# Optimization experiments

Measured on AMD Instinct MI355X. Metric: run time of the kernel, lower is better.

Reference implementation:

```python
import jax, jax.numpy as jnp
import numpy as np

B, H, N, M = 8192, 512, 1024, 128
EPS_COS = 1e-8   # torch cosine_similarity default eps
EPS_NORM = 1e-16 # normalization eps in forward


def _linear_params(key, fan_in, fan_out):
    # torch nn.Linear default init: U(-1/sqrt(fan_in), 1/sqrt(fan_in))
    lim = 1.0 / np.sqrt(fan_in)
    kw, kb = jax.random.split(key)
    W = jax.random.uniform(kw, (fan_out, fan_in), minval=-lim, maxval=lim, dtype=jnp.float32)
    b = jax.random.uniform(kb, (fan_out,), minval=-lim, maxval=lim, dtype=jnp.float32)
    return W, b


def setup_inputs() -> dict:
    key = jax.random.key(0)
    ks = jax.random.split(key, 8)
    Wk, bk = _linear_params(ks[0], H, M)
    Wb, bb = _linear_params(ks[1], H, 1)
    Wg, bg = _linear_params(ks[2], H, 1)
    Ws, bs = _linear_params(ks[3], H, N)
    Wgam, bgam = _linear_params(ks[4], H, 1)
    x = jax.random.normal(ks[5], (B, H), dtype=jnp.float32)
    # previous_state is an attention-weight vector over memory rows (sums to 1)
    previous_state = jax.nn.softmax(jax.random.normal(ks[6], (B, N), dtype=jnp.float32), axis=-1)
    memory = jax.random.normal(ks[7], (N, M), dtype=jnp.float32)
    return dict(x=x, previous_state=previous_state, memory=memory,
                Wk=Wk, bk=bk, Wb=Wb, bb=bb, Wg=Wg, bg=bg,
                Ws=Ws, bs=bs, Wgam=Wgam, bgam=bgam)


def _circular_convolution(w, s):
    # Full circular convolution over the memory axis:
    #   out[b, i] = sum_j w[b, j] * s[b, (i - j) mod N]
    # Implemented via FFT to avoid materializing a [B, N, N] shift matrix.
    out = jnp.fft.irfft(jnp.fft.rfft(w, axis=-1) * jnp.fft.rfft(s, axis=-1),
                        n=w.shape[-1], axis=-1)
    # conv of nonnegative weights is nonnegative; clamp tiny FFT round-off
    # negatives so the fractional power below stays well defined.
    return jnp.maximum(out, 0.0)


def reference(x, previous_state, memory, Wk, bk, Wb, bb, Wg, bg, Ws, bs, Wgam, bgam):
    k = x @ Wk.T + bk                                   # [B, M]
    beta = jax.nn.softplus(x @ Wb.T + bb)               # [B, 1]
    g = jax.nn.sigmoid(x @ Wg.T + bg)                   # [B, 1]
    s = jax.nn.softmax(x @ Ws.T + bs, axis=-1)          # [B, N]
    gamma = 1.0 + jax.nn.softplus(x @ Wgam.T + bgam)    # [B, 1]

    # cosine similarity between each key and each memory row -> [B, N]
    k_n = k / jnp.maximum(jnp.linalg.norm(k, axis=-1, keepdims=True), EPS_COS)
    m_n = memory / jnp.maximum(jnp.linalg.norm(memory, axis=-1, keepdims=True), EPS_COS)
    cos = k_n @ m_n.T                                   # [B, N]

    w_c = jax.nn.softmax(beta * cos, axis=1)            # content addressing
    w_g = g * w_c + (1.0 - g) * previous_state          # interpolation gate
    w_t = _circular_convolution(w_g, s)                 # location shift
    w = w_t ** gamma                                    # sharpening
    w = w / (jnp.sum(w, axis=1, keepdims=True) + EPS_NORM)

    read = w @ memory                                   # [B, M]
    return read, w
```

## Files before the change

kernel.cpp:

```cpp
#include <hip/hip_runtime.h>
#include <hip/hip_bf16.h>

typedef __attribute__((ext_vector_type(8))) short short8;
typedef __attribute__((ext_vector_type(4))) short short4v;
typedef __attribute__((ext_vector_type(4))) float f32x4;

#define B_ROWS 8192
#define HDIM 512
#define NDIM 1024
#define MDIM 128

__device__ __forceinline__ float softplusf(float z) {
  return fmaxf(z, 0.f) + log1pf(__expf(-fabsf(z)));
}
__device__ __forceinline__ unsigned short f2bfu(float f) {
  __hip_bfloat16 h = __float2bfloat16(f);
  return *reinterpret_cast<unsigned short*>(&h);
}
__device__ __forceinline__ short8 pack8(float4 a, float4 b) {
  short8 r;
  r[0] = (short)f2bfu(a.x); r[1] = (short)f2bfu(a.y);
  r[2] = (short)f2bfu(a.z); r[3] = (short)f2bfu(a.w);
  r[4] = (short)f2bfu(b.x); r[5] = (short)f2bfu(b.y);
  r[6] = (short)f2bfu(b.z); r[7] = (short)f2bfu(b.w);
  return r;
}
__device__ __forceinline__ int pad(int i) { return i + (i >> 4); }

__global__ __launch_bounds__(256) void prep_all(
    const float* __restrict__ x, const float* __restrict__ Ws,
    const float* __restrict__ Wk, const float* __restrict__ mem,
    const float* __restrict__ Wb, const float* __restrict__ bb,
    const float* __restrict__ Wg, const float* __restrict__ bg,
    const float* __restrict__ Wgam, const float* __restrict__ bgam,
    short* __restrict__ xb, short* __restrict__ wsb, short* __restrict__ wkb,
    short* __restrict__ mn_bf, short* __restrict__ memT_bf,
    float* __restrict__ bgg)
{
  const int blk = blockIdx.x, t = threadIdx.x;
  if (blk < 512) {
    __shared__ float sredp[4];
    const int half = t >> 7, tl = t & 127;
    const int n = blk * 2 + half;
    const int wid = t >> 6;
    const float v = mem[n * MDIM + tl];
    float ss = v * v;
#pragma unroll
    for (int o = 32; o; o >>= 1) ss += __shfl_xor(ss, o);
    if ((t & 63) == 0) sredp[wid] = ss;
    __syncthreads();
    const float inv = 1.f / fmaxf(sqrtf(sredp[half * 2] + sredp[half * 2 + 1]), 1e-8f);
    mn_bf[n * MDIM + tl] = (short)f2bfu(v * inv);
    memT_bf[(size_t)tl * NDIM + n] = (short)f2bfu(v);
  } else if (blk < 2560) {
    const int wid = t >> 6, lane = t & 63;
    const int b = (blk - 512) * 4 + wid;
    const size_t xo = (size_t)b * HDIM + lane * 8;
    const float4 x0 = *(const float4*)(x + xo);
    const float4 x1 = *(const float4*)(x + xo + 4);
    const float4 b0 = *(const float4*)(Wb + lane * 8);
    const float4 b1 = *(const float4*)(Wb + lane * 8 + 4);
    const float4 g0 = *(const float4*)(Wg + lane * 8);
    const float4 g1 = *(const float4*)(Wg + lane * 8 + 4);
    const float4 m0 = *(const float4*)(Wgam + lane * 8);
    const float4 m1 = *(const float4*)(Wgam + lane * 8 + 4);
    float zb = x0.x*b0.x + x0.y*b0.y + x0.z*b0.z + x0.w*b0.w
             + x1.x*b1.x + x1.y*b1.y + x1.z*b1.z + x1.w*b1.w;
    float zg = x0.x*g0.x + x0.y*g0.y + x0.z*g0.z + x0.w*g0.w
             + x1.x*g1.x + x1.y*g1.y + x1.z*g1.z + x1.w*g1.w;
    float zm = x0.x*m0.x + x0.y*m0.y + x0.z*m0.z + x0.w*m0.w
             + x1.x*m1.x + x1.y*m1.y + x1.z*m1.z + x1.w*m1.w;
#pragma unroll
    for (int o = 32; o; o >>= 1) {
      zb += __shfl_xor(zb, o); zg += __shfl_xor(zg, o); zm += __shfl_xor(zm, o);
    }
    if (lane == 0) {
      zb += bb[0]; zg += bg[0]; zm += bgam[0];
      bgg[b * 4 + 0] = softplusf(zb);
      bgg[b * 4 + 1] = 1.f / (1.f + __expf(-zg));
      bgg[b * 4 + 2] = 1.f + softplusf(zm);
    }
  } else {
    const int NX = B_ROWS * HDIM / 4;
    const int NS = NDIM * HDIM / 4;
    const int NK = MDIM * HDIM / 4;
    const int stride = 1024 * 256;
    for (int i = (blk - 2560) * 256 + t; i < NX + NS + NK; i += stride) {
      const float* src; short* dst; int j = i;
      if (j < NX) { src = x; dst = xb; }
      else if (j < NX + NS) { j -= NX; src = Ws; dst = wsb; }
      else { j -= NX + NS; src = Wk; dst = wkb; }
      const float4 v = ((const float4*)src)[j];
      short4v o;
      o[0] = (short)f2bfu(v.x); o[1] = (short)f2bfu(v.y);
      o[2] = (short)f2bfu(v.z); o[3] = (short)f2bfu(v.w);
      ((short4v*)dst)[j] = o;
    }
  }
}

__global__ __launch_bounds__(256) void kgemm_norm(
    const short* __restrict__ xb, const short* __restrict__ wkb,
    const float* __restrict__ bk, short* __restrict__ khat)
{
  __shared__ __align__(16) short sA[32][40];
  __shared__ __align__(16) short sW[128][40];
  __shared__ float snorm[4][32];
  __shared__ float sinv[32];

  const int tid = threadIdx.x, lane = tid & 63, wid = tid >> 6;
  const int bm = blockIdx.x;
  const int fr = lane & 15, kg = (lane >> 4) << 3;

  f32x4 acc[2][2] = {};

  for (int k0 = 0; k0 < HDIM; k0 += 32) {
    if (k0) __syncthreads();
    if (tid < 128) {
      const int row = tid >> 2, c0 = (tid & 3) * 8;
      *(short8*)(&sA[row][c0]) =
          *(const short8*)(xb + (size_t)(bm * 32 + row) * HDIM + k0 + c0);
    }
#pragma unroll
    for (int u = tid; u < 512; u += 256) {
      const int row = u >> 2, c0 = (u & 3) * 8;
      *(short8*)(&sW[row][c0]) =
          *(const short8*)(wkb + (size_t)row * HDIM + k0 + c0);
    }
    __syncthreads();

    short8 af[2], bf[2];
#pragma unroll
    for (int i = 0; i < 2; i++) af[i] = *(const short8*)(&sA[i * 16 + fr][kg]);
#pragma unroll
    for (int n = 0; n < 2; n++) bf[n] = *(const short8*)(&sW[wid * 32 + n * 16 + fr][kg]);
#pragma unroll
    for (int i = 0; i < 2; i++)
#pragma unroll
      for (int n = 0; n < 2; n++)
        acc[i][n] = __builtin_amdgcn_mfma_f32_16x16x32_bf16(af[i], bf[n], acc[i][n], 0, 0, 0);
  }

  const int rbase = (lane >> 4) << 2;
  float z[2][2][4];
#pragma unroll
  for (int i = 0; i < 2; i++)
#pragma unroll
    for (int n = 0; n < 2; n++) {
      const float bv = bk[wid * 32 + n * 16 + fr];
#pragma unroll
      for (int r = 0; r < 4; r++) z[i][n][r] = acc[i][n][r] + bv;
    }
#pragma unroll
  for (int i = 0; i < 2; i++)
#pragma unroll
    for (int r = 0; r < 4; r++) {
      float sq = z[i][0][r] * z[i][0][r] + z[i][1][r] * z[i][1][r];
      sq += __shfl_xor(sq, 1); sq += __shfl_xor(sq, 2);
      sq += __shfl_xor(sq, 4); sq += __shfl_xor(sq, 8);
      if (fr == 0) snorm[wid][i * 16 + rbase + r] = sq;
    }
  __syncthreads();
  if (tid < 32) {
    const float nn = snorm[0][tid] + snorm[1][tid] + snorm[2][tid] + snorm[3][tid];
    sinv[tid] = 1.f / fmaxf(sqrtf(nn), 1e-8f);
  }
  __syncthreads();
#pragma unroll
  for (int i = 0; i < 2; i++)
#pragma unroll
    for (int n = 0; n < 2; n++)
#pragma unroll
      for (int r = 0; r < 4; r++) {
        const int grl = i * 16 + rbase + r;
        khat[(size_t)(bm * 32 + grl) * MDIM + wid * 32 + n * 16 + fr] =
            (short)f2bfu(z[i][n][r] * sinv[grl]);
      }
}

template<bool AF32, bool WF32>
__global__ __launch_bounds__(256) void gemm_bt(
    const void* __restrict__ Av, const void* __restrict__ Wv,
    const float* __restrict__ bias, float* __restrict__ C,
    int ncols, int K)
{
  __shared__ __align__(16) short sA[64][40];
  __shared__ __align__(16) short sW[64][40];

  const int tid = threadIdx.x;
  const int bm = blockIdx.y, bn = blockIdx.x;
  const int lrow = tid >> 2;
  const int lcol = (tid & 3) << 3;
  const int wid = tid >> 6, lane = tid & 63;
  const int wr = wid >> 1, wc = wid & 1;
  const int fr = lane & 15, kg = (lane >> 4) << 3;

  f32x4 acc[2][2] = {};

  const size_t arow = (size_t)(bm * 64 + lrow) * K + lcol;
  const size_t wrow = (size_t)(bn * 64 + lrow) * K + lcol;

  for (int k0 = 0; k0 < K; k0 += 32) {
    if constexpr (AF32) {
      const float* A = (const float*)Av;
      const float4 a0 = *(const float4*)(A + arow + k0);
      const float4 a1 = *(const float4*)(A + arow + k0 + 4);
      *(short8*)(&sA[lrow][lcol]) = pack8(a0, a1);
    } else {
      const short* A = (const short*)Av;
      *(short8*)(&sA[lrow][lcol]) = *(const short8*)(A + arow + k0);
    }
    if constexpr (WF32) {
      const float* W = (const float*)Wv;
      const float4 w0 = *(const float4*)(W + wrow + k0);
      const float4 w1 = *(const float4*)(W + wrow + k0 + 4);
      *(short8*)(&sW[lrow][lcol]) = pack8(w0, w1);
    } else {
      const short* W = (const short*)Wv;
      *(short8*)(&sW[lrow][lcol]) = *(const short8*)(W + wrow + k0);
    }
    __syncthreads();

    short8 af[2], bf[2];
#pragma unroll
    for (int i = 0; i < 2; i++) af[i] = *(const short8*)(&sA[wr * 32 + i * 16 + fr][kg]);
#pragma unroll
    for (int n = 0; n < 2; n++) bf[n] = *(const short8*)(&sW[wc * 32 + n * 16 + fr][kg]);

#pragma unroll
    for (int i = 0; i < 2; i++)
#pragma unroll
      for (int n = 0; n < 2; n++)
        acc[i][n] = __builtin_amdgcn_mfma_f32_16x16x32_bf16(af[i], bf[n], acc[i][n], 0, 0, 0);
    __syncthreads();
  }

#pragma unroll
  for (int i = 0; i < 2; i++)
#pragma unroll
    for (int n = 0; n < 2; n++) {
      const int gr = bm * 64 + wr * 32 + i * 16 + ((lane >> 4) << 2);
      const int gc = bn * 64 + wc * 32 + n * 16 + fr;
      const float bv = bias ? bias[gc] : 0.f;
#pragma unroll
      for (int r = 0; r < 4; r++)
        C[(size_t)(gr + r) * ncols + gc] = acc[i][n][r] + bv;
    }
}

template<bool AF32, bool WF32>
__global__ __launch_bounds__(256) void kgemm128(
    const void* __restrict__ Av, const void* __restrict__ Wv,
    const float* __restrict__ bias, float* __restrict__ C,
    int ncols, int K)
{
  __shared__ __align__(16) short sA[128 * 32];
  __shared__ __align__(16) short sB[128 * 32];

  const int tid = threadIdx.x, lane = tid & 63, wid = tid >> 6;
  const int bm = blockIdx.y, bn = blockIdx.x;
  const int wr = wid >> 1, wc = wid & 1;
  const int fr = lane & 15, kg = (lane >> 4) << 3;

  f32x4 acc[4][4] = {};

  for (int k0 = 0; k0 < K; k0 += 32) {
    if (k0) __syncthreads();

    if constexpr (AF32) {
      const float* A = (const float*)Av;
      const int row = tid >> 1, c0 = (tid & 1) * 16;
      const float* src = A + (size_t)(bm * 128 + row) * K + k0 + c0;
      const float4 v0 = *(const float4*)src;
      const float4 v1 = *(const float4*)(src + 4);
      const float4 v2 = *(const float4*)(src + 8);
      const float4 v3 = *(const float4*)(src + 12);
      short* d = &sA[row * 32 + c0];
      *(short8*)d = pack8(v0, v1);
      *(short8*)(d + 8) = pack8(v2, v3);
    } else {
      const short* A = (const short*)Av;
#pragma unroll
      for (int j = 0; j < 2; j++) {
        const int c = tid + j * 256;
        const short* g = A + (size_t)(bm * 128 + (c >> 2)) * K + k0 + (c & 3) * 8;
        short* l = &sA[(j * 256 + wid * 64) * 8];
        __builtin_amdgcn_global_load_lds(
            (const __attribute__((address_space(1))) void*)g,
            (__attribute__((address_space(3))) void*)l, 16, 0, 0);
      }
    }

    if constexpr (WF32) {
      const float* W = (const float*)Wv;
      const int row = tid >> 1, c0 = (tid & 1) * 16;
      const float* src = W + (size_t)(bn * 128 + row) * K + k0 + c0;
      const float4 v0 = *(const float4*)src;
      const float4 v1 = *(const float4*)(src + 4);
      const float4 v2 = *(const float4*)(src + 8);
      const float4 v3 = *(const float4*)(src + 12);
      short* d = &sB[row * 32 + c0];
      *(short8*)d = pack8(v0, v1);
      *(short8*)(d + 8) = pack8(v2, v3);
    } else {
      const short* W = (const short*)Wv;
#pragma unroll
      for (int j = 0; j < 2; j++) {
        const int c = tid + j * 256;
        const short* g = W + (size_t)(bn * 128 + (c >> 2)) * K + k0 + (c & 3) * 8;
        short* l = &sB[(j * 256 + wid * 64) * 8];
        __builtin_amdgcn_global_load_lds(
            (const __attribute__((address_space(1))) void*)g,
            (__attribute__((address_space(3))) void*)l, 16, 0, 0);
      }
    }
    __syncthreads();

    short8 af[4], bf[4];
#pragma unroll
    for (int m = 0; m < 4; m++)
      af[m] = *(const short8*)(&sA[(wr * 64 + m * 16 + fr) * 32 + kg]);
#pragma unroll
    for (int n = 0; n < 4; n++)
      bf[n] = *(const short8*)(&sB[(wc * 64 + n * 16 + fr) * 32 + kg]);

#pragma unroll
    for (int m = 0; m < 4; m++)
#pragma unroll
      for (int n = 0; n < 4; n++)
        acc[m][n] = __builtin_amdgcn_mfma_f32_16x16x32_bf16(af[m], bf[n], acc[m][n], 0, 0, 0);
  }

#pragma unroll
  for (int m = 0; m < 4; m++)
#pragma unroll
    for (int n = 0; n < 4; n++) {
      const int gr = bm * 128 + wr * 64 + m * 16 + ((lane >> 4) << 2);
      const int gc = bn * 128 + wc * 64 + n * 16 + fr;
      const float bv = bias ? bias[gc] : 0.f;
#pragma unroll
      for (int r = 0; r < 4; r++)
        C[(size_t)(gr + r) * ncols + gc] = acc[m][n][r] + bv;
    }
}

#define ANG0 (-0.0061359231515425650f)

template<int ST>
__device__ __forceinline__ void fft_mid(const float* __restrict__ sr,
                                        const float* __restrict__ si,
                                        float* __restrict__ dr,
                                        float* __restrict__ di, int tid,
                                        int j0, int j1, int j2, int j3)
{
  const int ls = 2 * ST, s = 1 << ls;
  const int p = tid >> ls, q = tid & (s - 1), tb = tid & ~(s - 1);
  const float a0r = sr[j0], a0i = si[j0], a1r = sr[j1], a1i = si[j1];
  const float a2r = sr[j2], a2i = si[j2], a3r = sr[j3], a3i = si[j3];
  const float b0r = a0r + a2r, b0i = a0i + a2i, b1r = a1r + a3r, b1i = a1i + a3i;
  const float b2r = a0r - a2r, b2i = a0i - a2i, b3r = a1r - a3r, b3i = a1i - a3i;
  const float A0r = b0r + b1r, A0i = b0i + b1i;
  const float A1r = b2r + b3i, A1i = b2i - b3r;
  const float A2r = b0r - b1r, A2i = b0i - b1i;
  const float A3r = b2r - b3i, A3i = b2i + b3r;
  const int o = q + 4 * s * p;
  dr[pad(o)] = A0r; di[pad(o)] = A0i;
  if constexpr (ST < 4) {
    float s1, c1; __sincosf(ANG0 * (float)tb, &s1, &c1);
    const float c2 = c1 * c1 - s1 * s1, s2 = 2.f * s1 * c1;
    const float c3 = c1 * c2 - s1 * s2, s3 = s1 * c2 + c1 * s2;
    dr[pad(o + s)]     = A1r * c1 - A1i * s1; di[pad(o + s)]     = A1r * s1 + A1i * c1;
    dr[pad(o + 2 * s)] = A2r * c2 - A2i * s2; di[pad(o + 2 * s)] = A2r * s2 + A2i * c2;
    dr[pad(o + 3 * s)] = A3r * c3 - A3i * s3; di[pad(o + 3 * s)] = A3r * s3 + A3i * c3;
  } else {
    dr[pad(o + s)]     = A1r; di[pad(o + s)]     = A1i;
    dr[pad(o + 2 * s)] = A2r; di[pad(o + 2 * s)] = A2i;
    dr[pad(o + 3 * s)] = A3r; di[pad(o + 3 * s)] = A3i;
  }
  __syncthreads();
}

template<int J>
__device__ __forceinline__ void fft512_mid(const float* __restrict__ sr,
                                           const float* __restrict__ si,
                                           float* __restrict__ dr,
                                           float* __restrict__ di, int tid)
{
  if (tid < 128) {
    constexpr int s  = (J == 1) ? 2 : (J == 2) ? 8 : 32;
    constexpr int ns = (J == 1) ? 256 : (J == 2) ? 64 : 16;
    constexpr int ls = (J == 1) ? 1 : (J == 2) ? 3 : 5;
    const int p = tid >> ls, q = tid & (s - 1);
    const float a0r = sr[pad(tid)],       a0i = si[pad(tid)];
    const float a1r = sr[pad(tid + 128)], a1i = si[pad(tid + 128)];
    const float a2r = sr[pad(tid + 256)], a2i = si[pad(tid + 256)];
    const float a3r = sr[pad(tid + 384)], a3i = si[pad(tid + 384)];
    const float b0r = a0r + a2r, b0i = a0i + a2i, b1r = a1r + a3r, b1i = a1i + a3i;
    const float b2r = a0r - a2r, b2i = a0i - a2i, b3r = a1r - a3r, b3i = a1i - a3i;
    const float A0r = b0r + b1r, A0i = b0i + b1i;
    const float A1r = b2r + b3i, A1i = b2i - b3r;
    const float A2r = b0r - b1r, A2i = b0i - b1i;
    const float A3r = b2r - b3i, A3i = b2i + b3r;
    float s1, c1; __sincosf((-6.283185307179586f / (float)ns) * (float)p, &s1, &c1);
    const float c2 = c1 * c1 - s1 * s1, s2 = 2.f * s1 * c1;
    const float c3 = c1 * c2 - s1 * s2, s3 = s1 * c2 + c1 * s2;
    const int o = q + 4 * s * p;
    dr[pad(o)]         = A0r;                 di[pad(o)]         = A0i;
    dr[pad(o + s)]     = A1r * c1 - A1i * s1; di[pad(o + s)]     = A1r * s1 + A1i * c1;
    dr[pad(o + 2 * s)] = A2r * c2 - A2i * s2; di[pad(o + 2 * s)] = A2r * s2 + A2i * c2;
    dr[pad(o + 3 * s)] = A3r * c3 - A3i * s3; di[pad(o + 3 * s)] = A3r * s3 + A3i * c3;
  }
  __syncthreads();
}

__global__ __launch_bounds__(256) void rowpass(
    const float* __restrict__ slog, const float* __restrict__ cosb,
    const float* __restrict__ bgg, const float* __restrict__ prev,
    float* __restrict__ wout)
{
  __shared__ float bAr[1088], bAi[1088], bBr[1088], bBi[1088];
  __shared__ float sred[8];
  const int b = blockIdx.x, tid = threadIdx.x;
  const int lane = tid & 63, wid = tid >> 6;
  const int j0 = pad(tid), j1 = pad(tid + 256), j2 = pad(tid + 512), j3 = pad(tid + 768);

  const float beta = bgg[b * 4 + 0], g = bgg[b * 4 + 1], gamma = bgg[b * 4 + 2];

  float sv[4], cv[4];
  float e1 = 0.f, e2 = 0.f;
#pragma unroll
  for (int i = 0; i < 4; i++) {
    sv[i] = __expf(slog[(size_t)b * NDIM + tid + i * 256]);
    cv[i] = __expf(beta * cosb[(size_t)b * NDIM + tid + i * 256]);
    e1 += sv[i]; e2 += cv[i];
  }
#pragma unroll
  for (int o = 32; o; o >>= 1) { e1 += __shfl_xor(e1, o); e2 += __shfl_xor(e2, o); }
  if (lane == 0) { sred[wid * 2] = e1; sred[wid * 2 + 1] = e2; }
  __syncthreads();
  const float r1 = 1.f / (sred[0] + sred[2] + sred[4] + sred[6]);
  const float r2 = 1.f / (sred[1] + sred[3] + sred[5] + sred[7]);

  float s1, c1; __sincosf(ANG0 * (float)tid, &s1, &c1);
  const float c2 = c1 * c1 - s1 * s1, s2 = 2.f * s1 * c1;
  const float c3 = c1 * c2 - s1 * s2, s3 = s1 * c2 + c1 * s2;

  {
    float ar[4], ai[4];
#pragma unroll
    for (int i = 0; i < 4; i++) {
      const int idx = tid + i * 256;
      const float pv = prev[(size_t)b * NDIM + idx];
      ar[i] = g * cv[i] * r2 + (1.f - g) * pv;
      ai[i] = sv[i] * r1;
    }
    const float b0r = ar[0] + ar[2], b0i = ai[0] + ai[2];
    const float b1r = ar[1] + ar[3], b1i = ai[1] + ai[3];
    const float b2r = ar[0] - ar[2], b2i = ai[0] - ai[2];
    const float b3r = ar[1] - ar[3], b3i = ai[1] - ai[3];
    const float A0r = b0r + b1r, A0i = b0i + b1i;
    const float A1r = b2r + b3i, A1i = b2i - b3r;
    const float A2r = b0r - b1r, A2i = b0i - b1i;
    const float A3r = b2r - b3i, A3i = b2i + b3r;
    const int o4 = 4 * tid;
    bBr[pad(o4)]     = A0r;                  bBi[pad(o4)]     = A0i;
    bBr[pad(o4 + 1)] = A1r * c1 - A1i * s1;  bBi[pad(o4 + 1)] = A1r * s1 + A1i * c1;
    bBr[pad(o4 + 2)] = A2r * c2 - A2i * s2;  bBi[pad(o4 + 2)] = A2r * s2 + A2i * c2;
    bBr[pad(o4 + 3)] = A3r * c3 - A3i * s3;  bBi[pad(o4 + 3)] = A3r * s3 + A3i * c3;
  }
  __syncthreads();

  fft_mid<1>(bBr, bBi, bAr, bAi, tid, j0, j1, j2, j3);
  fft_mid<2>(bAr, bAi, bBr, bBi, tid, j0, j1, j2, j3);
  fft_mid<3>(bBr, bBi, bAr, bAi, tid, j0, j1, j2, j3);
  fft_mid<4>(bAr, bAi, bBr, bBi, tid, j0, j1, j2, j3);

#pragma unroll
  for (int i = 0; i < 2; i++) {
    const int k = tid + i * 256;
    const int kp = pad(k), rp = pad((1024 - k) & 1023);
    const float Zkr = bBr[kp], Zki = bBi[kp];
    const float Zrr = bBr[rp], Zri = bBi[rp];
    const float Wr = 0.5f * (Zkr + Zrr), Wi = 0.5f * (Zki - Zri);
    const float Sr = 0.5f * (Zki + Zri), Si = 0.5f * (Zrr - Zkr);
    bAr[kp] = Wr * Sr - Wi * Si;
    bAi[kp] = Wr * Si + Wi * Sr;
  }
  if (tid == 0) {
    const int kp = pad(512);
    bAr[kp] = bBr[kp] * bBi[kp];
    bAi[kp] = 0.f;
  }
  __syncthreads();

  {
    float es, ec; __sincosf(0.0061359231515425650f * (float)tid, &es, &ec);
    const float P0r = bAr[pad(tid)],       P0i = bAi[pad(tid)];
    const float Pa0r = bAr[pad(512 - tid)], Pa0i = bAi[pad(512 - tid)];
    const float S0r = P0r + Pa0r, S0i = P0i - Pa0i;
    const float D0r = P0r - Pa0r, D0i = P0i + Pa0i;
    const float Q0r = S0r - es * D0r - ec * D0i;
    const float Q0i = S0i + ec * D0r - es * D0i;
    const float P1r = bAr[pad(tid + 256)],  P1i = bAi[pad(tid + 256)];
    const float Pa1r = bAr[pad(256 - tid)], Pa1i = bAi[pad(256 - tid)];
    const float S1r = P1r + Pa1r, S1i = P1i - Pa1i;
    const float D1r = P1r - Pa1r, D1i = P1i + Pa1i;
    const float Q1r = S1r - ec * D1r + es * D1i;
    const float Q1i = S1i - es * D1r - ec * D1i;
    const float ur = Q0r, ui = -Q0i, vr = Q1r, vi = -Q1i;
    float ts, tc; __sincosf(-0.012271846303085130f * (float)tid, &ts, &tc);
    const float d_r = ur - vr, d_i = ui - vi;
    bBr[pad(2 * tid)]     = ur + vr;             bBi[pad(2 * tid)]     = ui + vi;
    bBr[pad(2 * tid + 1)] = d_r * tc - d_i * ts; bBi[pad(2 * tid + 1)] = d_r * ts + d_i * tc;
  }
  __syncthreads();

  fft512_mid<1>(bBr, bBi, bAr, bAi, tid);
  fft512_mid<2>(bAr, bAi, bBr, bBi, tid);
  fft512_mid<3>(bBr, bBi, bAr, bAi, tid);

  if (tid < 128) {
    const int i0 = pad(tid), i1 = pad(tid + 128), i2 = pad(tid + 256), i3 = pad(tid + 384);
    const float a0r = bAr[i0], a0i = bAi[i0], a1r = bAr[i1], a1i = bAi[i1];
    const float a2r = bAr[i2], a2i = bAi[i2], a3r = bAr[i3], a3i = bAi[i3];
    const float b0r = a0r + a2r, b0i = a0i + a2i, b1r = a1r + a3r, b1i = a1i + a3i;
    const float b2r = a0r - a2r, b2i = a0i - a2i, b3r = a1r - a3r, b3i = a1i - a3i;
    bBr[i0] = b0r + b1r; bBi[i0] = b0i + b1i;
    bBr[i1] = b2r + b3i; bBi[i1] = b2i - b3r;
    bBr[i2] = b0r - b1r; bBi[i2] = b0i - b1i;
    bBr[i3] = b2r - b3i; bBi[i3] = b2i + b3r;
  }
  __syncthreads();

  const int m0 = pad(2 * tid), m1 = pad(2 * tid + 1);
  float xv[4];
  xv[0] =  bBr[m0] * (1.f / 1024.f);
  xv[1] = -bBi[m0] * (1.f / 1024.f);
  xv[2] =  bBr[m1] * (1.f / 1024.f);
  xv[3] = -bBi[m1] * (1.f / 1024.f);

  float wt[4]; float esum = 0.f;
#pragma unroll
  for (int i = 0; i < 4; i++) {
    const float v = fmaxf(xv[i], 0.f);
    const float p = (v > 0.f) ? __expf(gamma * __logf(v)) : 0.f;
    wt[i] = p; esum += p;
  }
#pragma unroll
  for (int o = 32; o; o >>= 1) esum += __shfl_xor(esum, o);
  if (lane == 0) sred[wid] = esum;
  __syncthreads();
  const float rn = 1.f / (sred[0] + sred[1] + sred[2] + sred[3] + 1e-16f);
  *(float4*)(wout + (size_t)b * NDIM + 4 * tid) =
      make_float4(wt[0] * rn, wt[1] * rn, wt[2] * rn, wt[3] * rn);
}

extern "C" void kernel_launch(void* const* d_in, const int* in_sizes, int n_in,
                              void* d_out, int out_size, void* d_ws, size_t ws_size,
                              hipStream_t stream)
{
  const float* x    = (const float*)d_in[0];
  const float* prev = (const float*)d_in[1];
  const float* mem  = (const float*)d_in[2];
  const float* Wk   = (const float*)d_in[3];
  const float* bk   = (const float*)d_in[4];
  const float* Wb   = (const float*)d_in[5];
  const float* bb   = (const float*)d_in[6];
  const float* Wg   = (const float*)d_in[7];
  const float* bg   = (const float*)d_in[8];
  const float* Ws   = (const float*)d_in[9];
  const float* bs   = (const float*)d_in[10];
  const float* Wgam = (const float*)d_in[11];
  const float* bgam = (const float*)d_in[12];

  char* ws = (char*)d_ws;
  short* mn_bf   = (short*)(ws + 0);
  short* memT_bf = (short*)(ws + 262144);
  short* khat    = (short*)(ws + 524288);
  float* bgg     = (float*)(ws + 2621440);
  float* slog    = (float*)(ws + 2752512);
  float* cosb    = (float*)(ws + 36306944);
  short* xb      = (short*)(ws + 36306944);
  short* wsb     = (short*)(ws + 44695552);
  short* wkb     = (short*)(ws + 45744128);

  float* readout = (float*)d_out;
  float* wout = readout + (size_t)B_ROWS * MDIM;

  prep_all<<<3584, 256, 0, stream>>>(x, Ws, Wk, mem, Wb, bb, Wg, bg, Wgam, bgam,
                                     xb, wsb, wkb, mn_bf, memT_bf, bgg);
  kgemm_norm<<<B_ROWS / 32, 256, 0, stream>>>(xb, wkb, bk, khat);
  kgemm128<false, false><<<dim3(NDIM / 128, B_ROWS / 128), 256, 0, stream>>>(
      xb, wsb, bs, slog, NDIM, HDIM);
  kgemm128<false, false><<<dim3(NDIM / 128, B_ROWS / 128), 256, 0, stream>>>(
      khat, mn_bf, nullptr, cosb, NDIM, MDIM);
  rowpass<<<B_ROWS, 256, 0, stream>>>(slog, cosb, bgg, prev, wout);
  gemm_bt<true, false><<<dim3(MDIM / 64, B_ROWS / 64), 256, 0, stream>>>(
      wout, memT_bf, nullptr, readout, MDIM, NDIM);
}
```

Baseline: 126.4 us.

## Fuse x bf16 cast into gate pass, table FFT twiddles, use bf16 weights for read GEMM

The x-to-bf16 conversion now happens in the blocks that already load x for the scalar gates, which shrinks the prep grid and avoids a second full read of x. The rowpass kernel builds a shared-memory twiddle table once per block and reads from it instead of calling sincos in every FFT stage. It also writes a bf16 copy of the final weights, so the read GEMM uses the 128x128 kgemm128 kernel on bf16 input instead of gemm_bt converting fp32 on the fly. The cost is an extra bf16 write of w, a workspace buffer, and a read GEMM with only 64 blocks, which may underfill the GPU.

```diff
diff --git a/kernel.cpp b/kernel.cpp
--- a/kernel.cpp
+++ b/kernel.cpp
@@ -58,6 +58,7 @@
     const size_t xo = (size_t)b * HDIM + lane * 8;
     const float4 x0 = *(const float4*)(x + xo);
     const float4 x1 = *(const float4*)(x + xo + 4);
+    *(short8*)(xb + xo) = pack8(x0, x1);
     const float4 b0 = *(const float4*)(Wb + lane * 8);
     const float4 b1 = *(const float4*)(Wb + lane * 8 + 4);
     const float4 g0 = *(const float4*)(Wg + lane * 8);
@@ -81,15 +82,13 @@
       bgg[b * 4 + 2] = 1.f + softplusf(zm);
     }
   } else {
-    const int NX = B_ROWS * HDIM / 4;
-    const int NS = NDIM * HDIM / 4;
-    const int NK = MDIM * HDIM / 4;
-    const int stride = 1024 * 256;
-    for (int i = (blk - 2560) * 256 + t; i < NX + NS + NK; i += stride) {
+    const int NS4 = NDIM * HDIM / 4;
+    const int NK4 = MDIM * HDIM / 4;
+    const int stride = 144 * 256;
+    for (int i = (blk - 2560) * 256 + t; i < NS4 + NK4; i += stride) {
       const float* src; short* dst; int j = i;
-      if (j < NX) { src = x; dst = xb; }
-      else if (j < NX + NS) { j -= NX; src = Ws; dst = wsb; }
-      else { j -= NX + NS; src = Wk; dst = wkb; }
+      if (j < NS4) { src = Ws; dst = wsb; }
+      else { j -= NS4; src = Wk; dst = wkb; }
       const float4 v = ((const float4*)src)[j];
       short4v o;
       o[0] = (short)f2bfu(v.x); o[1] = (short)f2bfu(v.y);
@@ -176,76 +175,6 @@
         khat[(size_t)(bm * 32 + grl) * MDIM + wid * 32 + n * 16 + fr] =
             (short)f2bfu(z[i][n][r] * sinv[grl]);
       }
-}
-
-template<bool AF32, bool WF32>
-__global__ __launch_bounds__(256) void gemm_bt(
-    const void* __restrict__ Av, const void* __restrict__ Wv,
-    const float* __restrict__ bias, float* __restrict__ C,
-    int ncols, int K)
-{
-  __shared__ __align__(16) short sA[64][40];
-  __shared__ __align__(16) short sW[64][40];
-
-  const int tid = threadIdx.x;
-  const int bm = blockIdx.y, bn = blockIdx.x;
-  const int lrow = tid >> 2;
-  const int lcol = (tid & 3) << 3;
-  const int wid = tid >> 6, lane = tid & 63;
-  const int wr = wid >> 1, wc = wid & 1;
-  const int fr = lane & 15, kg = (lane >> 4) << 3;
-
-  f32x4 acc[2][2] = {};
-
-  const size_t arow = (size_t)(bm * 64 + lrow) * K + lcol;
-  const size_t wrow = (size_t)(bn * 64 + lrow) * K + lcol;
-
-  for (int k0 = 0; k0 < K; k0 += 32) {
-    if constexpr (AF32) {
-      const float* A = (const float*)Av;
-      const float4 a0 = *(const float4*)(A + arow + k0);
-      const float4 a1 = *(const float4*)(A + arow + k0 + 4);
-      *(short8*)(&sA[lrow][lcol]) = pack8(a0, a1);
-    } else {
-      const short* A = (const short*)Av;
-      *(short8*)(&sA[lrow][lcol]) = *(const short8*)(A + arow + k0);
-    }
-    if constexpr (WF32) {
-      const float* W = (const float*)Wv;
-      const float4 w0 = *(const float4*)(W + wrow + k0);
-      const float4 w1 = *(const float4*)(W + wrow + k0 + 4);
-      *(short8*)(&sW[lrow][lcol]) = pack8(w0, w1);
-    } else {
-      const short* W = (const short*)Wv;
-      *(short8*)(&sW[lrow][lcol]) = *(const short8*)(W + wrow + k0);
-    }
-    __syncthreads();
-
-    short8 af[2], bf[2];
-#pragma unroll
-    for (int i = 0; i < 2; i++) af[i] = *(const short8*)(&sA[wr * 32 + i * 16 + fr][kg]);
-#pragma unroll
-    for (int n = 0; n < 2; n++) bf[n] = *(const short8*)(&sW[wc * 32 + n * 16 + fr][kg]);
-
-#pragma unroll
-    for (int i = 0; i < 2; i++)
-#pragma unroll
-      for (int n = 0; n < 2; n++)
-        acc[i][n] = __builtin_amdgcn_mfma_f32_16x16x32_bf16(af[i], bf[n], acc[i][n], 0, 0, 0);
-    __syncthreads();
-  }
-
-#pragma unroll
-  for (int i = 0; i < 2; i++)
-#pragma unroll
-    for (int n = 0; n < 2; n++) {
-      const int gr = bm * 64 + wr * 32 + i * 16 + ((lane >> 4) << 2);
-      const int gc = bn * 64 + wc * 32 + n * 16 + fr;
-      const float bv = bias ? bias[gc] : 0.f;
-#pragma unroll
-      for (int r = 0; r < 4; r++)
-        C[(size_t)(gr + r) * ncols + gc] = acc[i][n][r] + bv;
-    }
 }
 
 template<bool AF32, bool WF32>
@@ -350,7 +279,9 @@
 __device__ __forceinline__ void fft_mid(const float* __restrict__ sr,
                                         const float* __restrict__ si,
                                         float* __restrict__ dr,
-                                        float* __restrict__ di, int tid,
+                                        float* __restrict__ di,
+                                        const float* __restrict__ twc,
+                                        const float* __restrict__ twn, int tid,
                                         int j0, int j1, int j2, int j3)
 {
   const int ls = 2 * ST, s = 1 << ls;
@@ -366,9 +297,9 @@
   const int o = q + 4 * s * p;
   dr[pad(o)] = A0r; di[pad(o)] = A0i;
   if constexpr (ST < 4) {
-    float s1, c1; __sincosf(ANG0 * (float)tb, &s1, &c1);
-    const float c2 = c1 * c1 - s1 * s1, s2 = 2.f * s1 * c1;
-    const float c3 = c1 * c2 - s1 * s2, s3 = s1 * c2 + c1 * s2;
+    const float c1 = twc[tb], s1 = twn[tb];
+    const float c2 = twc[2 * tb], s2 = twn[2 * tb];
+    const float c3 = c2 * c1 - s2 * s1, s3 = s2 * c1 + c2 * s1;
     dr[pad(o + s)]     = A1r * c1 - A1i * s1; di[pad(o + s)]     = A1r * s1 + A1i * c1;
     dr[pad(o + 2 * s)] = A2r * c2 - A2i * s2; di[pad(o + 2 * s)] = A2r * s2 + A2i * c2;
     dr[pad(o + 3 * s)] = A3r * c3 - A3i * s3; di[pad(o + 3 * s)] = A3r * s3 + A3i * c3;
@@ -384,11 +315,13 @@
 __device__ __forceinline__ void fft512_mid(const float* __restrict__ sr,
                                            const float* __restrict__ si,
                                            float* __restrict__ dr,
-                                           float* __restrict__ di, int tid)
+                                           float* __restrict__ di,
+                                           const float* __restrict__ twc,
+                                           const float* __restrict__ twn, int tid)
 {
   if (tid < 128) {
     constexpr int s  = (J == 1) ? 2 : (J == 2) ? 8 : 32;
-    constexpr int ns = (J == 1) ? 256 : (J == 2) ? 64 : 16;
+    constexpr int tm = (J == 1) ? 4 : (J == 2) ? 16 : 64;
     constexpr int ls = (J == 1) ? 1 : (J == 2) ? 3 : 5;
     const int p = tid >> ls, q = tid & (s - 1);
     const float a0r = sr[pad(tid)],       a0i = si[pad(tid)];
@@ -401,9 +334,9 @@
     const float A1r = b2r + b3i, A1i = b2i - b3r;
     const float A2r = b0r - b1r, A2i = b0i - b1i;
     const float A3r = b2r - b3i, A3i = b2i + b3r;
-    float s1, c1; __sincosf((-6.283185307179586f / (float)ns) * (float)p, &s1, &c1);
-    const float c2 = c1 * c1 - s1 * s1, s2 = 2.f * s1 * c1;
-    const float c3 = c1 * c2 - s1 * s2, s3 = s1 * c2 + c1 * s2;
+    const float c1 = twc[tm * p], s1 = twn[tm * p];
+    const float c2 = twc[2 * tm * p], s2 = twn[2 * tm * p];
+    const float c3 = c2 * c1 - s2 * s1, s3 = s2 * c1 + c2 * s1;
     const int o = q + 4 * s * p;
     dr[pad(o)]         = A0r;                 di[pad(o)]         = A0i;
     dr[pad(o + s)]     = A1r * c1 - A1i * s1; di[pad(o + s)]     = A1r * s1 + A1i * c1;
@@ -416,14 +349,20 @@
 __global__ __launch_bounds__(256) void rowpass(
     const float* __restrict__ slog, const float* __restrict__ cosb,
     const float* __restrict__ bgg, const float* __restrict__ prev,
-    float* __restrict__ wout)
+    float* __restrict__ wout, short* __restrict__ wbf)
 {
   __shared__ float bAr[1088], bAi[1088], bBr[1088], bBi[1088];
+  __shared__ float twc[512], twn[512];
   __shared__ float sred[8];
   const int b = blockIdx.x, tid = threadIdx.x;
   const int lane = tid & 63, wid = tid >> 6;
   const int j0 = pad(tid), j1 = pad(tid + 256), j2 = pad(tid + 512), j3 = pad(tid + 768);
 
+  for (int i = tid; i < 512; i += 256) {
+    float sn, cs; __sincosf(ANG0 * (float)i, &sn, &cs);
+    twc[i] = cs; twn[i] = sn;
+  }
+
   const float beta = bgg[b * 4 + 0], g = bgg[b * 4 + 1], gamma = bgg[b * 4 + 2];
 
   float sv[4], cv[4];
@@ -441,9 +380,12 @@
   const float r1 = 1.f / (sred[0] + sred[2] + sred[4] + sred[6]);
   const float r2 = 1.f / (sred[1] + sred[3] + sred[5] + sred[7]);
 
-  float s1, c1; __sincosf(ANG0 * (float)tid, &s1, &c1);
-  const float c2 = c1 * c1 - s1 * s1, s2 = 2.f * s1 * c1;
-  const float c3 = c1 * c2 - s1 * s2, s3 = s1 * c2 + c1 * s2;
+  const float c1 = twc[tid], s1 = twn[tid];
+  const float c2 = twc[2 * tid >= 512 ? 2 * tid - 512 : 2 * tid] * (2 * tid >= 512 ? -1.f : 1.f),
+              s2x = twn[2 * tid >= 512 ? 2 * tid - 512 : 2 * tid] * (2 * tid >= 512 ? -1.f : 1.f);
+  const float c2_ = twc[2 * tid], s2_ = twn[2 * tid];
+  const float c3 = c2_ * c1 - s2_ * s1, s3 = s2_ * c1 + c2_ * s1;
+  (void)c2; (void)s2x;
 
   {
     float ar[4], ai[4];
@@ -463,17 +405,17 @@
     const float A2r = b0r - b1r, A2i = b0i - b1i;
     const float A3r = b2r - b3i, A3i = b2i + b3r;
     const int o4 = 4 * tid;
-    bBr[pad(o4)]     = A0r;                  bBi[pad(o4)]     = A0i;
-    bBr[pad(o4 + 1)] = A1r * c1 - A1i * s1;  bBi[pad(o4 + 1)] = A1r * s1 + A1i * c1;
-    bBr[pad(o4 + 2)] = A2r * c2 - A2i * s2;  bBi[pad(o4 + 2)] = A2r * s2 + A2i * c2;
-    bBr[pad(o4 + 3)] = A3r * c3 - A3i * s3;  bBi[pad(o4 + 3)] = A3r * s3 + A3i * c3;
-  }
-  __syncthreads();
-
-  fft_mid<1>(bBr, bBi, bAr, bAi, tid, j0, j1, j2, j3);
-  fft_mid<2>(bAr, bAi, bBr, bBi, tid, j0, j1, j2, j3);
-  fft_mid<3>(bBr, bBi, bAr, bAi, tid, j0, j1, j2, j3);
-  fft_mid<4>(bAr, bAi, bBr, bBi, tid, j0, j1, j2, j3);
+    bBr[pad(o4)]     = A0r;                    bBi[pad(o4)]     = A0i;
+    bBr[pad(o4 + 1)] = A1r * c1 - A1i * s1;    bBi[pad(o4 + 1)] = A1r * s1 + A1i * c1;
+    bBr[pad(o4 + 2)] = A2r * c2_ - A2i * s2_;  bBi[pad(o4 + 2)] = A2r * s2_ + A2i * c2_;
+    bBr[pad(o4 + 3)] = A3r * c3 - A3i * s3;    bBi[pad(o4 + 3)] = A3r * s3 + A3i * c3;
+  }
+  __syncthreads();
+
+  fft_mid<1>(bBr, bBi, bAr, bAi, twc, twn, tid, j0, j1, j2, j3);
+  fft_mid<2>(bAr, bAi, bBr, bBi, twc, twn, tid, j0, j1, j2, j3);
+  fft_mid<3>(bBr, bBi, bAr, bAi, twc, twn, tid, j0, j1, j2, j3);
+  fft_mid<4>(bAr, bAi, bBr, bBi, twc, twn, tid, j0, j1, j2, j3);
 
 #pragma unroll
   for (int i = 0; i < 2; i++) {
@@ -494,8 +436,8 @@
   __syncthreads();
 
   {
-    float es, ec; __sincosf(0.0061359231515425650f * (float)tid, &es, &ec);
-    const float P0r = bAr[pad(tid)],       P0i = bAi[pad(tid)];
+    const float ec = twc[tid], es = -twn[tid];
+    const float P0r = bAr[pad(tid)],        P0i = bAi[pad(tid)];
     const float Pa0r = bAr[pad(512 - tid)], Pa0i = bAi[pad(512 - tid)];
     const float S0r = P0r + Pa0r, S0i = P0i - Pa0i;
     const float D0r = P0r - Pa0r, D0i = P0i + Pa0i;
@@ -508,16 +450,16 @@
     const float Q1r = S1r - ec * D1r + es * D1i;
     const float Q1i = S1i - es * D1r - ec * D1i;
     const float ur = Q0r, ui = -Q0i, vr = Q1r, vi = -Q1i;
-    float ts, tc; __sincosf(-0.012271846303085130f * (float)tid, &ts, &tc);
+    const float tc = twc[2 * tid], ts = twn[2 * tid];
     const float d_r = ur - vr, d_i = ui - vi;
     bBr[pad(2 * tid)]     = ur + vr;             bBi[pad(2 * tid)]     = ui + vi;
     bBr[pad(2 * tid + 1)] = d_r * tc - d_i * ts; bBi[pad(2 * tid + 1)] = d_r * ts + d_i * tc;
   }
   __syncthreads();
 
-  fft512_mid<1>(bBr, bBi, bAr, bAi, tid);
-  fft512_mid<2>(bAr, bAi, bBr, bBi, tid);
-  fft512_mid<3>(bBr, bBi, bAr, bAi, tid);
+  fft512_mid<1>(bBr, bBi, bAr, bAi, twc, twn, tid);
+  fft512_mid<2>(bAr, bAi, bBr, bBi, twc, twn, tid);
+  fft512_mid<3>(bBr, bBi, bAr, bAi, twc, twn, tid);
 
   if (tid < 128) {
     const int i0 = pad(tid), i1 = pad(tid + 128), i2 = pad(tid + 256), i3 = pad(tid + 384);
@@ -551,8 +493,12 @@
   if (lane == 0) sred[wid] = esum;
   __syncthreads();
   const float rn = 1.f / (sred[0] + sred[1] + sred[2] + sred[3] + 1e-16f);
-  *(float4*)(wout + (size_t)b * NDIM + 4 * tid) =
-      make_float4(wt[0] * rn, wt[1] * rn, wt[2] * rn, wt[3] * rn);
+  const float w0 = wt[0] * rn, w1 = wt[1] * rn, w2 = wt[2] * rn, w3 = wt[3] * rn;
+  *(float4*)(wout + (size_t)b * NDIM + 4 * tid) = make_float4(w0, w1, w2, w3);
+  short4v wb;
+  wb[0] = (short)f2bfu(w0); wb[1] = (short)f2bfu(w1);
+  wb[2] = (short)f2bfu(w2); wb[3] = (short)f2bfu(w3);
+  *(short4v*)(wbf + (size_t)b * NDIM + 4 * tid) = wb;
 }
 
 extern "C" void kernel_launch(void* const* d_in, const int* in_sizes, int n_in,
@@ -583,18 +529,19 @@
   short* xb      = (short*)(ws + 36306944);
   short* wsb     = (short*)(ws + 44695552);
   short* wkb     = (short*)(ws + 45744128);
+  short* wbf     = (short*)(ws + 69861376);
 
   float* readout = (float*)d_out;
   float* wout = readout + (size_t)B_ROWS * MDIM;
 
-  prep_all<<<3584, 256, 0, stream>>>(x, Ws, Wk, mem, Wb, bb, Wg, bg, Wgam, bgam,
+  prep_all<<<2704, 256, 0, stream>>>(x, Ws, Wk, mem, Wb, bb, Wg, bg, Wgam, bgam,
                                      xb, wsb, wkb, mn_bf, memT_bf, bgg);
   kgemm_norm<<<B_ROWS / 32, 256, 0, stream>>>(xb, wkb, bk, khat);
   kgemm128<false, false><<<dim3(NDIM / 128, B_ROWS / 128), 256, 0, stream>>>(
       xb, wsb, bs, slog, NDIM, HDIM);
   kgemm128<false, false><<<dim3(NDIM / 128, B_ROWS / 128), 256, 0, stream>>>(
       khat, mn_bf, nullptr, cosb, NDIM, MDIM);
-  rowpass<<<B_ROWS, 256, 0, stream>>>(slog, cosb, bgg, prev, wout);
-  gemm_bt<true, false><<<dim3(MDIM / 64, B_ROWS / 64), 256, 0, stream>>>(
-      wout, memT_bf, nullptr, readout, MDIM, NDIM);
-}
+  rowpass<<<B_ROWS, 256, 0, stream>>>(slog, cosb, bgg, prev, wout, wbf);
+  kgemm128<false, false><<<dim3(1, B_ROWS / 128), 256, 0, stream>>>(
+      wbf, memT_bf, nullptr, readout, MDIM, NDIM);
+}
```

Result: slower. 130.4 us (+3.2%).
